# Kernel tuning notes

Measured on AMD Instinct MI355X. Metric: run time of the kernel, lower is better.

The kernel has to match this reference:

```python
import jax, jax.numpy as jnp
import numpy as np


def setup_inputs() -> dict:
    key = jax.random.key(0)
    ks = jax.random.split(key, 7)
    B, Q, K, D, H = 4, 256, 1024, 512, 128
    return {
        "queries": jax.random.normal(ks[0], (B, Q, D), dtype=jnp.float32),
        "keys": jax.random.normal(ks[1], (B, K, D), dtype=jnp.float32),
        "values": jax.random.normal(ks[2], (B, K, D), dtype=jnp.float32),
        "Wq": jax.random.normal(ks[3], (D, H), dtype=jnp.float32) * (1.0 / np.sqrt(D)),
        "Wk": jax.random.normal(ks[4], (D, H), dtype=jnp.float32) * (1.0 / np.sqrt(D)),
        "wv": jax.random.normal(ks[5], (H,), dtype=jnp.float32) * (1.0 / np.sqrt(H)),
        "valid_lens": jax.random.randint(ks[6], (B,), 1, K + 1, dtype=jnp.int32),
    }


def reference(queries, keys, values, Wq, Wk, wv, valid_lens):
    # queries: (B,Q,D), keys/values: (B,K,D)
    q = jnp.einsum("bqd,dh->bqh", queries, Wq)
    k = jnp.einsum("bkd,dh->bkh", keys, Wk)
    # broadcast-add -> (B,Q,K,H), tanh, project with wv -> scores (B,Q,K)
    features = jnp.tanh(q[:, :, None, :] + k[:, None, :, :])
    scores = jnp.einsum("bqkh,h->bqk", features, wv)
    # masked softmax: original replaces masked logits with 0 (not -inf)
    K_len = keys.shape[1]
    mask = jnp.arange(K_len)[None, None, :] < valid_lens[:, None, None]  # (B,1,K)
    masked = jnp.where(mask, scores, 0.0)
    attn = jax.nn.softmax(masked, axis=-1)
    # dropout is identity at inference
    return jnp.einsum("bqk,bkd->bqd", attn, values)
```

## Files before the change

kernel.cpp:

```cpp
#include <hip/hip_runtime.h>

#define NB 4
#define NQ 256
#define NK 1024
#define ND 512
#define NH 128

typedef _Float16 half8_t __attribute__((ext_vector_type(8)));
typedef _Float16 half4_t __attribute__((ext_vector_type(4)));
typedef _Float16 half2_t __attribute__((ext_vector_type(2)));
typedef float f32x4_t __attribute__((ext_vector_type(4)));

#define TANH_C 2.8853900817779268f

__global__ __launch_bounds__(256) void prep_kernel(
    const float* __restrict__ Wq, const float* __restrict__ Wk,
    const float* __restrict__ values, _Float16* __restrict__ WQT,
    _Float16* __restrict__ WKT, _Float16* __restrict__ vT) {
  __shared__ float smem[64 * 130];
  const int bid = blockIdx.x;
  const int t = threadIdx.x;

  if (bid < 16) {
    float(*tile)[129] = (float(*)[129])smem;
    const float* W = (bid >= 8) ? Wk : Wq;
    _Float16* WT = (bid >= 8) ? WKT : WQT;
    const int d0 = (bid & 7) * 64;
    #pragma unroll
    for (int j = 0; j < 32; ++j) {
      const int idx = t + j * 256;
      tile[idx >> 7][idx & 127] = W[(size_t)(d0 + (idx >> 7)) * NH + (idx & 127)];
    }
    __syncthreads();
    #pragma unroll
    for (int j = 0; j < 32; ++j) {
      const int idx = t + j * 256;
      const int h = idx >> 6, r = idx & 63;
      WT[(size_t)h * ND + d0 + r] = (_Float16)tile[r][h];
    }
    return;
  }

  const int vb = bid - 16;
  float(*tile)[65] = (float(*)[65])smem;
  const int dt = vb & 7;
  const int kt = (vb >> 3) & 15;
  const int b = vb >> 7;
  const int k0 = kt * 64, d0 = dt * 64;
  {
    const int kl = t >> 4, dl4 = (t & 15) * 4;
    #pragma unroll
    for (int i = 0; i < 4; ++i) {
      const float4 v = *(const float4*)(
          values + ((size_t)(b * NK + k0 + kl + i * 16)) * ND + d0 + dl4);
      tile[dl4 + 0][kl + i * 16] = v.x;
      tile[dl4 + 1][kl + i * 16] = v.y;
      tile[dl4 + 2][kl + i * 16] = v.z;
      tile[dl4 + 3][kl + i * 16] = v.w;
    }
  }
  __syncthreads();
  const int dr = t >> 2, kc = (t & 3) * 16;
  half8_t h0, h1;
  #pragma unroll
  for (int ii = 0; ii < 8; ++ii) {
    h0[ii] = (_Float16)tile[dr][kc + ii];
    h1[ii] = (_Float16)tile[dr][kc + 8 + ii];
  }
  _Float16* dst = vT + ((size_t)(b * ND + d0 + dr)) * NK + k0 + kc;
  *(half8_t*)dst = h0;
  *(half8_t*)(dst + 8) = h1;
}

__global__ __launch_bounds__(256) void proj_mfma_kernel(
    const float* __restrict__ queries, const float* __restrict__ keys,
    const _Float16* __restrict__ WQT, const _Float16* __restrict__ WKT,
    float* __restrict__ EQ, float* __restrict__ EKT) {
  const int bid = blockIdx.x;
  const int row0 = bid * 16;
  const bool is_q = row0 < NB * NQ;
  const float* X = is_q ? queries : (keys - (size_t)NB * NQ * ND);
  const _Float16* WT = is_q ? WQT : WKT;

  const int w = threadIdx.x >> 6;
  const int l = threadIdx.x & 63;
  const int h0 = w * 32;

  const float* xrow = X + (size_t)(row0 + (l & 15)) * ND + (l >> 4) * 8;
  const _Float16* wt0 = WT + (size_t)(h0 + (l & 15)) * ND + (l >> 4) * 8;
  const _Float16* wt1 = wt0 + 16 * ND;

  f32x4_t acc0 = {0.f, 0.f, 0.f, 0.f};
  f32x4_t acc1 = {0.f, 0.f, 0.f, 0.f};
  #pragma unroll 4
  for (int d = 0; d < ND; d += 32) {
    const float4 x0 = *(const float4*)(xrow + d);
    const float4 x1 = *(const float4*)(xrow + d + 4);
    half8_t a;
    a[0] = (_Float16)x0.x; a[1] = (_Float16)x0.y;
    a[2] = (_Float16)x0.z; a[3] = (_Float16)x0.w;
    a[4] = (_Float16)x1.x; a[5] = (_Float16)x1.y;
    a[6] = (_Float16)x1.z; a[7] = (_Float16)x1.w;
    const half8_t b0 = *(const half8_t*)(wt0 + d);
    const half8_t b1 = *(const half8_t*)(wt1 + d);
    acc0 = __builtin_amdgcn_mfma_f32_16x16x32_f16(a, b0, acc0, 0, 0, 0);
    acc1 = __builtin_amdgcn_mfma_f32_16x16x32_f16(a, b1, acc1, 0, 0, 0);
  }
  const int mrow = row0 + (l >> 4) * 4;
  const int hcol = h0 + (l & 15);
  if (is_q) {
    #pragma unroll
    for (int r = 0; r < 4; ++r) {
      EQ[(size_t)(mrow + r) * NH + hcol] = __builtin_exp2f(TANH_C * acc0[r]);
      EQ[(size_t)(mrow + r) * NH + hcol + 16] = __builtin_exp2f(TANH_C * acc1[r]);
    }
  } else {
    const int rowk = mrow - NB * NQ;
    const int bb = rowk >> 10;
    const int kk = rowk & 1023;
    float4 v0, v1;
    v0.x = __builtin_exp2f(TANH_C * acc0[0]);
    v0.y = __builtin_exp2f(TANH_C * acc0[1]);
    v0.z = __builtin_exp2f(TANH_C * acc0[2]);
    v0.w = __builtin_exp2f(TANH_C * acc0[3]);
    v1.x = __builtin_exp2f(TANH_C * acc1[0]);
    v1.y = __builtin_exp2f(TANH_C * acc1[1]);
    v1.z = __builtin_exp2f(TANH_C * acc1[2]);
    v1.w = __builtin_exp2f(TANH_C * acc1[3]);
    *(float4*)(EKT + ((size_t)(bb * NH + hcol)) * NK + kk) = v0;
    *(float4*)(EKT + ((size_t)(bb * NH + hcol + 16)) * NK + kk) = v1;
  }
}

__global__ __launch_bounds__(512, 4) void scores_softmax_kernel(
    const float* __restrict__ EQ, const float* __restrict__ EKT,
    const float* __restrict__ wv, const int* __restrict__ vlen,
    _Float16* __restrict__ attn_h) {
  __shared__ float4 eqwv2[2][64];
  __shared__ float red[2][2][8];
  const int bid = blockIdx.x;
  const int b = bid >> 7;
  const int q0 = (bid & 127) * 2;
  const int t = threadIdx.x;
  const int w = t >> 6;
  const int l = t & 63;
  const int vl = vlen[b];

  if (t < 128) {
    const int qq = t >> 6, i = t & 63;
    const float* eqrow = EQ + (size_t)(b * NQ + q0 + qq) * NH;
    eqwv2[qq][i] = make_float4(eqrow[2 * i], wv[2 * i],
                               eqrow[2 * i + 1], wv[2 * i + 1]);
  }
  __syncthreads();

  float Wsum;
  {
    const float4 a = eqwv2[0][l];
    Wsum = a.y + a.w;
    #pragma unroll
    for (int off = 32; off; off >>= 1) Wsum += __shfl_xor(Wsum, off);
  }

  const int k0 = w * 128;
  float a00 = 0.f, a01 = 0.f, a10 = 0.f, a11 = 0.f;
  if (k0 < vl) {
    const float* ekb = EKT + (size_t)(b * NH) * NK + k0 + l * 2;
    #pragma unroll 4
    for (int hh = 0; hh < 64; ++hh) {
      const float4 qw0 = eqwv2[0][hh];
      const float4 qw1 = eqwv2[1][hh];
      const float2 ea = *(const float2*)(ekb + (size_t)(2 * hh) * NK);
      const float2 eb = *(const float2*)(ekb + (size_t)(2 * hh + 1) * NK);
      {
        const float da = fmaf(qw0.x, ea.x, 1.f), db = fmaf(qw0.z, eb.x, 1.f);
        a00 = fmaf(fmaf(qw0.y, db, qw0.w * da),
                   __builtin_amdgcn_rcpf(da * db), a00);
      }
      {
        const float da = fmaf(qw0.x, ea.y, 1.f), db = fmaf(qw0.z, eb.y, 1.f);
        a01 = fmaf(fmaf(qw0.y, db, qw0.w * da),
                   __builtin_amdgcn_rcpf(da * db), a01);
      }
      {
        const float da = fmaf(qw1.x, ea.x, 1.f), db = fmaf(qw1.z, eb.x, 1.f);
        a10 = fmaf(fmaf(qw1.y, db, qw1.w * da),
                   __builtin_amdgcn_rcpf(da * db), a10);
      }
      {
        const float da = fmaf(qw1.x, ea.y, 1.f), db = fmaf(qw1.z, eb.y, 1.f);
        a11 = fmaf(fmaf(qw1.y, db, qw1.w * da),
                   __builtin_amdgcn_rcpf(da * db), a11);
      }
    }
  }

  const int kA = k0 + l * 2, kB = kA + 1;
  float s00 = (kA < vl) ? (Wsum - 2.f * a00) : 0.f;
  float s01 = (kB < vl) ? (Wsum - 2.f * a01) : 0.f;
  float s10 = (kA < vl) ? (Wsum - 2.f * a10) : 0.f;
  float s11 = (kB < vl) ? (Wsum - 2.f * a11) : 0.f;

  float m0 = fmaxf(s00, s01), m1 = fmaxf(s10, s11);
  #pragma unroll
  for (int off = 32; off; off >>= 1) {
    m0 = fmaxf(m0, __shfl_xor(m0, off));
    m1 = fmaxf(m1, __shfl_xor(m1, off));
  }
  if (l == 0) { red[0][0][w] = m0; red[0][1][w] = m1; }
  __syncthreads();
  m0 = red[0][0][0]; m1 = red[0][1][0];
  #pragma unroll
  for (int i = 1; i < 8; ++i) {
    m0 = fmaxf(m0, red[0][0][i]);
    m1 = fmaxf(m1, red[0][1][i]);
  }
  const float ce = 1.4426950408889634f;
  s00 = __builtin_exp2f(ce * (s00 - m0));
  s01 = __builtin_exp2f(ce * (s01 - m0));
  s10 = __builtin_exp2f(ce * (s10 - m1));
  s11 = __builtin_exp2f(ce * (s11 - m1));
  float sum0 = s00 + s01, sum1 = s10 + s11;
  #pragma unroll
  for (int off = 32; off; off >>= 1) {
    sum0 += __shfl_xor(sum0, off);
    sum1 += __shfl_xor(sum1, off);
  }
  if (l == 0) { red[1][0][w] = sum0; red[1][1][w] = sum1; }
  __syncthreads();
  float Z0 = 0.f, Z1 = 0.f;
  #pragma unroll
  for (int i = 0; i < 8; ++i) { Z0 += red[1][0][i]; Z1 += red[1][1][i]; }
  const float inv0 = 1.0f / Z0, inv1 = 1.0f / Z1;
  half2_t h0, h1;
  h0[0] = (_Float16)(s00 * inv0); h0[1] = (_Float16)(s01 * inv0);
  h1[0] = (_Float16)(s10 * inv1); h1[1] = (_Float16)(s11 * inv1);
  *(half2_t*)(attn_h + (size_t)(b * NQ + q0) * NK + kA) = h0;
  *(half2_t*)(attn_h + (size_t)(b * NQ + q0 + 1) * NK + kA) = h1;
}

__global__ __launch_bounds__(256) void pv_mfma_kernel(
    const _Float16* __restrict__ attn_h, const _Float16* __restrict__ vT,
    float* __restrict__ out) {
  const int bid = blockIdx.x;
  const int dt = bid & 7;
  const int qt = (bid >> 3) & 15;
  const int b  = bid >> 7;
  const int w = threadIdx.x >> 6;
  const int l = threadIdx.x & 63;
  const int q_lo = qt * 16;
  const int d_lo = dt * 64 + w * 16;

  const _Float16* arow =
      attn_h + ((size_t)(b * NQ + q_lo + (l & 15))) * NK + (l >> 4) * 8;
  const _Float16* brow =
      vT + ((size_t)(b * ND + d_lo + (l & 15))) * NK + (l >> 4) * 8;

  f32x4_t acc = {0.f, 0.f, 0.f, 0.f};
  #pragma unroll 8
  for (int ks = 0; ks < NK; ks += 32) {
    const half8_t a = *(const half8_t*)(arow + ks);
    const half8_t bb = *(const half8_t*)(brow + ks);
    acc = __builtin_amdgcn_mfma_f32_16x16x32_f16(a, bb, acc, 0, 0, 0);
  }
  const int mrow = q_lo + (l >> 4) * 4;
  const int dcol = d_lo + (l & 15);
  #pragma unroll
  for (int r = 0; r < 4; ++r)
    out[(size_t)(b * NQ + mrow + r) * ND + dcol] = acc[r];
}

extern "C" void kernel_launch(void* const* d_in, const int* in_sizes, int n_in,
                              void* d_out, int out_size, void* d_ws, size_t ws_size,
                              hipStream_t stream) {
  const float* queries = (const float*)d_in[0];
  const float* keys    = (const float*)d_in[1];
  const float* values  = (const float*)d_in[2];
  const float* Wq      = (const float*)d_in[3];
  const float* Wk      = (const float*)d_in[4];
  const float* wv      = (const float*)d_in[5];
  const int*   vlen    = (const int*)d_in[6];
  float* out = (float*)d_out;

  char* ws = (char*)d_ws;
  float*     EQ     = (float*)(ws);
  float*     EKT    = (float*)(ws + (512 << 10));
  _Float16*  attn_h = (_Float16*)(ws + (2560 << 10));
  _Float16*  vT     = (_Float16*)(ws + (4608 << 10));
  _Float16*  WQT    = (_Float16*)(ws + (8704 << 10));
  _Float16*  WKT    = (_Float16*)(ws + (8832 << 10));

  prep_kernel<<<528, 256, 0, stream>>>(Wq, Wk, values, WQT, WKT, vT);
  proj_mfma_kernel<<<(NB * NQ + NB * NK) / 16, 256, 0, stream>>>(
      queries, keys, WQT, WKT, EQ, EKT);
  scores_softmax_kernel<<<NB * (NQ / 2), 512, 0, stream>>>(EQ, EKT, wv, vlen,
                                                           attn_h);
  pv_mfma_kernel<<<NB * 16 * 8, 256, 0, stream>>>(attn_h, vT, out);
}
```

Before: 58.40 us.

## Fuse weight transpose into projection kernel and merge with V transpose launch

```diff
diff --git a/kernel.cpp b/kernel.cpp
--- a/kernel.cpp
+++ b/kernel.cpp
@@ -13,35 +13,92 @@
 
 #define TANH_C 2.8853900817779268f
 
-__global__ __launch_bounds__(256) void prep_kernel(
+__global__ __launch_bounds__(256) void projvt_kernel(
+    const float* __restrict__ queries, const float* __restrict__ keys,
     const float* __restrict__ Wq, const float* __restrict__ Wk,
-    const float* __restrict__ values, _Float16* __restrict__ WQT,
-    _Float16* __restrict__ WKT, _Float16* __restrict__ vT) {
-  __shared__ float smem[64 * 130];
+    const float* __restrict__ values, float* __restrict__ EQ,
+    float* __restrict__ EKT, _Float16* __restrict__ vT) {
+  __shared__ __align__(16) char smem[33280];
   const int bid = blockIdx.x;
   const int t = threadIdx.x;
 
-  if (bid < 16) {
-    float(*tile)[129] = (float(*)[129])smem;
-    const float* W = (bid >= 8) ? Wk : Wq;
-    _Float16* WT = (bid >= 8) ? WKT : WQT;
-    const int d0 = (bid & 7) * 64;
-    #pragma unroll
-    for (int j = 0; j < 32; ++j) {
-      const int idx = t + j * 256;
-      tile[idx >> 7][idx & 127] = W[(size_t)(d0 + (idx >> 7)) * NH + (idx & 127)];
+  if (bid < 320) {
+    _Float16* wlds = (_Float16*)smem;
+    const int hgrp = bid & 3;
+    const int rblk = bid >> 2;
+    const int row0_blk = rblk * 64;
+    const bool is_q = row0_blk < NB * NQ;
+    const float* X = is_q ? queries : (keys - (size_t)NB * NQ * ND);
+    const float* W = is_q ? Wq : Wk;
+    const int h0 = hgrp * 32;
+
+    {
+      const int j = t & 31;
+      const int dg = t >> 5;
+      const int jx = (j & 7) << 3;
+      #pragma unroll 8
+      for (int pass = 0; pass < 64; ++pass) {
+        const int d = pass * 8 + dg;
+        wlds[j * 520 + (d ^ jx)] = (_Float16)W[(size_t)d * NH + h0 + j];
+      }
     }
     __syncthreads();
-    #pragma unroll
-    for (int j = 0; j < 32; ++j) {
-      const int idx = t + j * 256;
-      const int h = idx >> 6, r = idx & 63;
-      WT[(size_t)h * ND + d0 + r] = (_Float16)tile[r][h];
+
+    const int w = t >> 6;
+    const int l = t & 63;
+    const int row0 = row0_blk + w * 16;
+    const float* xrow = X + (size_t)(row0 + (l & 15)) * ND + (l >> 4) * 8;
+    const int hA = l & 15;
+    const int xorA = (hA & 7) << 3;
+
+    f32x4_t acc0 = {0.f, 0.f, 0.f, 0.f};
+    f32x4_t acc1 = {0.f, 0.f, 0.f, 0.f};
+    #pragma unroll 4
+    for (int d = 0; d < ND; d += 32) {
+      const float4 x0 = *(const float4*)(xrow + d);
+      const float4 x1 = *(const float4*)(xrow + d + 4);
+      half8_t a;
+      a[0] = (_Float16)x0.x; a[1] = (_Float16)x0.y;
+      a[2] = (_Float16)x0.z; a[3] = (_Float16)x0.w;
+      a[4] = (_Float16)x1.x; a[5] = (_Float16)x1.y;
+      a[6] = (_Float16)x1.z; a[7] = (_Float16)x1.w;
+      const int dfrag = d + (l >> 4) * 8;
+      const half8_t b0 =
+          *(const half8_t*)&wlds[hA * 520 + (dfrag ^ xorA)];
+      const half8_t b1 =
+          *(const half8_t*)&wlds[(16 + hA) * 520 + (dfrag ^ xorA)];
+      acc0 = __builtin_amdgcn_mfma_f32_16x16x32_f16(a, b0, acc0, 0, 0, 0);
+      acc1 = __builtin_amdgcn_mfma_f32_16x16x32_f16(a, b1, acc1, 0, 0, 0);
+    }
+    const int mrow = row0 + (l >> 4) * 4;
+    const int hcol = h0 + hA;
+    if (is_q) {
+      #pragma unroll
+      for (int r = 0; r < 4; ++r) {
+        EQ[(size_t)(mrow + r) * NH + hcol] = __builtin_exp2f(TANH_C * acc0[r]);
+        EQ[(size_t)(mrow + r) * NH + hcol + 16] =
+            __builtin_exp2f(TANH_C * acc1[r]);
+      }
+    } else {
+      const int rowk = mrow - NB * NQ;
+      const int bb = rowk >> 10;
+      const int kk = rowk & 1023;
+      float4 v0, v1;
+      v0.x = __builtin_exp2f(TANH_C * acc0[0]);
+      v0.y = __builtin_exp2f(TANH_C * acc0[1]);
+      v0.z = __builtin_exp2f(TANH_C * acc0[2]);
+      v0.w = __builtin_exp2f(TANH_C * acc0[3]);
+      v1.x = __builtin_exp2f(TANH_C * acc1[0]);
+      v1.y = __builtin_exp2f(TANH_C * acc1[1]);
+      v1.z = __builtin_exp2f(TANH_C * acc1[2]);
+      v1.w = __builtin_exp2f(TANH_C * acc1[3]);
+      *(float4*)(EKT + ((size_t)(bb * NH + hcol)) * NK + kk) = v0;
+      *(float4*)(EKT + ((size_t)(bb * NH + hcol + 16)) * NK + kk) = v1;
     }
     return;
   }
 
-  const int vb = bid - 16;
+  const int vb = bid - 320;
   float(*tile)[65] = (float(*)[65])smem;
   const int dt = vb & 7;
   const int kt = (vb >> 3) & 15;
@@ -61,75 +118,15 @@
   }
   __syncthreads();
   const int dr = t >> 2, kc = (t & 3) * 16;
-  half8_t h0, h1;
+  half8_t h0v, h1v;
   #pragma unroll
   for (int ii = 0; ii < 8; ++ii) {
-    h0[ii] = (_Float16)tile[dr][kc + ii];
-    h1[ii] = (_Float16)tile[dr][kc + 8 + ii];
+    h0v[ii] = (_Float16)tile[dr][kc + ii];
+    h1v[ii] = (_Float16)tile[dr][kc + 8 + ii];
   }
   _Float16* dst = vT + ((size_t)(b * ND + d0 + dr)) * NK + k0 + kc;
-  *(half8_t*)dst = h0;
-  *(half8_t*)(dst + 8) = h1;
-}
-
-__global__ __launch_bounds__(256) void proj_mfma_kernel(
-    const float* __restrict__ queries, const float* __restrict__ keys,
-    const _Float16* __restrict__ WQT, const _Float16* __restrict__ WKT,
-    float* __restrict__ EQ, float* __restrict__ EKT) {
-  const int bid = blockIdx.x;
-  const int row0 = bid * 16;
-  const bool is_q = row0 < NB * NQ;
-  const float* X = is_q ? queries : (keys - (size_t)NB * NQ * ND);
-  const _Float16* WT = is_q ? WQT : WKT;
-
-  const int w = threadIdx.x >> 6;
-  const int l = threadIdx.x & 63;
-  const int h0 = w * 32;
-
-  const float* xrow = X + (size_t)(row0 + (l & 15)) * ND + (l >> 4) * 8;
-  const _Float16* wt0 = WT + (size_t)(h0 + (l & 15)) * ND + (l >> 4) * 8;
-  const _Float16* wt1 = wt0 + 16 * ND;
-
-  f32x4_t acc0 = {0.f, 0.f, 0.f, 0.f};
-  f32x4_t acc1 = {0.f, 0.f, 0.f, 0.f};
-  #pragma unroll 4
-  for (int d = 0; d < ND; d += 32) {
-    const float4 x0 = *(const float4*)(xrow + d);
-    const float4 x1 = *(const float4*)(xrow + d + 4);
-    half8_t a;
-    a[0] = (_Float16)x0.x; a[1] = (_Float16)x0.y;
-    a[2] = (_Float16)x0.z; a[3] = (_Float16)x0.w;
-    a[4] = (_Float16)x1.x; a[5] = (_Float16)x1.y;
-    a[6] = (_Float16)x1.z; a[7] = (_Float16)x1.w;
-    const half8_t b0 = *(const half8_t*)(wt0 + d);
-    const half8_t b1 = *(const half8_t*)(wt1 + d);
-    acc0 = __builtin_amdgcn_mfma_f32_16x16x32_f16(a, b0, acc0, 0, 0, 0);
-    acc1 = __builtin_amdgcn_mfma_f32_16x16x32_f16(a, b1, acc1, 0, 0, 0);
-  }
-  const int mrow = row0 + (l >> 4) * 4;
-  const int hcol = h0 + (l & 15);
-  if (is_q) {
-    #pragma unroll
-    for (int r = 0; r < 4; ++r) {
-      EQ[(size_t)(mrow + r) * NH + hcol] = __builtin_exp2f(TANH_C * acc0[r]);
-      EQ[(size_t)(mrow + r) * NH + hcol + 16] = __builtin_exp2f(TANH_C * acc1[r]);
-    }
-  } else {
-    const int rowk = mrow - NB * NQ;
-    const int bb = rowk >> 10;
-    const int kk = rowk & 1023;
-    float4 v0, v1;
-    v0.x = __builtin_exp2f(TANH_C * acc0[0]);
-    v0.y = __builtin_exp2f(TANH_C * acc0[1]);
-    v0.z = __builtin_exp2f(TANH_C * acc0[2]);
-    v0.w = __builtin_exp2f(TANH_C * acc0[3]);
-    v1.x = __builtin_exp2f(TANH_C * acc1[0]);
-    v1.y = __builtin_exp2f(TANH_C * acc1[1]);
-    v1.z = __builtin_exp2f(TANH_C * acc1[2]);
-    v1.w = __builtin_exp2f(TANH_C * acc1[3]);
-    *(float4*)(EKT + ((size_t)(bb * NH + hcol)) * NK + kk) = v0;
-    *(float4*)(EKT + ((size_t)(bb * NH + hcol + 16)) * NK + kk) = v1;
-  }
+  *(half8_t*)dst = h0v;
+  *(half8_t*)(dst + 8) = h1v;
 }
 
 __global__ __launch_bounds__(512, 4) void scores_softmax_kernel(
@@ -287,12 +284,9 @@
   float*     EKT    = (float*)(ws + (512 << 10));
   _Float16*  attn_h = (_Float16*)(ws + (2560 << 10));
   _Float16*  vT     = (_Float16*)(ws + (4608 << 10));
-  _Float16*  WQT    = (_Float16*)(ws + (8704 << 10));
-  _Float16*  WKT    = (_Float16*)(ws + (8832 << 10));
-
-  prep_kernel<<<528, 256, 0, stream>>>(Wq, Wk, values, WQT, WKT, vT);
-  proj_mfma_kernel<<<(NB * NQ + NB * NK) / 16, 256, 0, stream>>>(
-      queries, keys, WQT, WKT, EQ, EKT);
+
+  projvt_kernel<<<832, 256, 0, stream>>>(queries, keys, Wq, Wk, values,
+                                         EQ, EKT, vT);
   scores_softmax_kernel<<<NB * (NQ / 2), 512, 0, stream>>>(EQ, EKT, wv, vlen,
                                                            attn_h);
   pv_mfma_kernel<<<NB * 16 * 8, 256, 0, stream>>>(attn_h, vT, out);
```

Result: faster. 54.17 us (-7.2%).
